# Optimization experiments

Measured on AMD Instinct MI355X. Metric: run time of the kernel, lower is better.

## Reference

```python
import jax, jax.numpy as jnp
import numpy as np

BN_EPS = 1e-5
MIN_DIST = 1e-10


def _conv_bn_relu(x, w, b, gamma, beta):
    # pointwise Conv1d (kernel=1) == per-point linear, then BatchNorm1d (training-mode
    # batch stats, biased variance, as torch does for normalization), then ReLU.
    y = jnp.einsum('oc,bcn->bon', w, x) + b[None, :, None]
    mu = y.mean(axis=(0, 2))
    var = y.var(axis=(0, 2))
    yn = (y - mu[None, :, None]) * jax.lax.rsqrt(var + BN_EPS)[None, :, None]
    return jax.nn.relu(yn * gamma[None, :, None] + beta[None, :, None])


def setup_inputs() -> dict:
    key = jax.random.key(0)
    ks = jax.random.split(key, 12)
    B, N1, N2, C1, C2 = 8, 8192, 2048, 128, 256
    in_ch = C1 + C2  # 384
    mlp = [256, 128]
    inp = {
        'xyz1': jax.random.normal(ks[0], (B, N1, 3), jnp.float32),
        'xyz2': jax.random.normal(ks[1], (B, N2, 3), jnp.float32),
        'points1': jax.random.normal(ks[2], (B, C1, N1), jnp.float32),
        'points2': jax.random.normal(ks[3], (B, C2, N2), jnp.float32),
    }
    last = in_ch
    for i, out_ch in enumerate(mlp):
        scale = 1.0 / np.sqrt(last)
        inp[f'w{i}'] = jax.random.uniform(ks[4 + 2 * i], (out_ch, last), jnp.float32, -scale, scale)
        inp[f'b{i}'] = jax.random.uniform(ks[5 + 2 * i], (out_ch,), jnp.float32, -scale, scale)
        inp[f'gamma{i}'] = jnp.ones((out_ch,), jnp.float32)
        inp[f'beta{i}'] = jnp.zeros((out_ch,), jnp.float32)
        last = out_ch
    return inp


def reference(xyz1, xyz2, points1, points2,
              w0, b0, gamma0, beta0, w1, b1, gamma1, beta1):
    # Euclidean distance matrix [B, N1, N2] (torch.cdist, p=2)
    sq = (jnp.sum(xyz1 * xyz1, -1)[:, :, None]
          + jnp.sum(xyz2 * xyz2, -1)[:, None, :]
          - 2.0 * jnp.einsum('bnd,bmd->bnm', xyz1, xyz2))
    dists = jnp.sqrt(jnp.maximum(sq, 0.0))
    # 3 smallest distances + indices (ascending, matching torch.topk largest=False)
    neg_d, knn_idx = jax.lax.top_k(-dists, 3)  # [B, N1, 3]
    knn_d = jnp.maximum(-neg_d, MIN_DIST)
    weights = 1.0 / knn_d
    weights = weights / jnp.sum(weights, axis=2, keepdims=True)  # [B, N1, 3]
    # gather neighbor features: points2 [B, C2, N2] -> [B, C2, N1, 3]
    knn_feats = jnp.take_along_axis(points2[:, :, None, :],
                                    knn_idx[:, None, :, :], axis=3)
    interpolated = jnp.sum(knn_feats * weights[:, None, :, :], axis=3)  # [B, C2, N1]
    new_points = jnp.concatenate([points1, interpolated], axis=1)  # [B, C1+C2, N1]
    new_points = _conv_bn_relu(new_points, w0, b0, gamma0, beta0)
    new_points = _conv_bn_relu(new_points, w1, b1, gamma1, beta1)
    return new_points
```

## Files before the change

### kernel.cpp

```cpp
#include <hip/hip_runtime.h>
#include <cstdint>

using u16 = unsigned short;
typedef short bf16x8 __attribute__((ext_vector_type(8)));
typedef float f32x4 __attribute__((ext_vector_type(4)));

__device__ __forceinline__ float bf2f(u16 h) {
    union { unsigned u; float f; } x;
    x.u = ((unsigned)h) << 16;
    return x.f;
}
__device__ __forceinline__ u16 f2bf(float f) {
    union { float f; unsigned u; } x;
    x.f = f;
    unsigned r = x.u + 0x7fffu + ((x.u >> 16) & 1u);
    return (u16)(r >> 16);
}

__device__ __forceinline__ void gl_lds16(const u16* g, u16* l) {
    __builtin_amdgcn_global_load_lds((const __attribute__((address_space(1))) void*)g,
                                     (__attribute__((address_space(3))) void*)l, 16, 0, 0);
}

#define N1 8192
#define N2 2048
#define C2 256

__global__ __launch_bounds__(256) void prep_misc(const float* __restrict__ w0,
                                                 const float* __restrict__ w1,
                                                 u16* __restrict__ w0b,
                                                 u16* __restrict__ w1b,
                                                 float* __restrict__ stats) {
    int bid = blockIdx.x, tid = threadIdx.x;
    if (bid < 384) {
        int i = bid * 256 + tid;
        w0b[i] = f2bf(w0[i]);
    } else if (bid < 512) {
        int i = (bid - 384) * 256 + tid;
        w1b[i] = f2bf(w1[i]);
    } else {
        for (int i = tid; i < 768; i += 256) stats[i] = 0.0f;
    }
}

__global__ __launch_bounds__(256) void transpose_to_bf16(const float* __restrict__ src,
                                                         u16* __restrict__ dst,
                                                         int C, int N, int dst_stride,
                                                         int col_off) {
    __shared__ float tile[32][33];
    int b = blockIdx.z;
    int n0 = blockIdx.x * 32, c0 = blockIdx.y * 32;
    int tx = threadIdx.x & 31, ty = threadIdx.x >> 5;
    const float* s = src + (long)b * C * N;
#pragma unroll
    for (int i = 0; i < 4; i++) {
        int c = ty + i * 8;
        tile[c][tx] = s[(long)(c0 + c) * N + n0 + tx];
    }
    __syncthreads();
    u16* d = dst + (long)b * N * dst_stride;
#pragma unroll
    for (int i = 0; i < 4; i++) {
        int n = ty + i * 8;
        d[(long)(n0 + n) * dst_stride + col_off + c0 + tx] = f2bf(tile[tx][n]);
    }
}

__global__ __launch_bounds__(256) void knn_interp(const float* __restrict__ xyz1,
                                                  const float* __restrict__ xyz2,
                                                  const u16* __restrict__ P2T,
                                                  u16* __restrict__ X) {
    __shared__ float4 pts[N2];
    __shared__ float m_d[4][64][3];
    __shared__ int   m_i[4][64][3];
    __shared__ int   s_idx[64][3];
    __shared__ float s_w[64][3];
    int b = blockIdx.y;
    int n0 = blockIdx.x * 64;
    int tid = threadIdx.x;
    int ql = tid & 63;
    int part = tid >> 6;

    for (int j = tid; j < N2; j += 256) {
        float x = xyz2[((long)b * N2 + j) * 3 + 0];
        float y = xyz2[((long)b * N2 + j) * 3 + 1];
        float z = xyz2[((long)b * N2 + j) * 3 + 2];
        float nsq = __fadd_rn(__fadd_rn(__fmul_rn(x, x), __fmul_rn(y, y)), __fmul_rn(z, z));
        pts[j] = make_float4(x, y, z, nsq);
    }
    __syncthreads();

    int n = n0 + ql;
    float px = xyz1[((long)b * N1 + n) * 3 + 0];
    float py = xyz1[((long)b * N1 + n) * 3 + 1];
    float pz = xyz1[((long)b * N1 + n) * 3 + 2];
    float psq = __fadd_rn(__fadd_rn(__fmul_rn(px, px), __fmul_rn(py, py)), __fmul_rn(pz, pz));

    float b0 = 1e30f, b1 = 1e30f, b2 = 1e30f;
    int i0 = 0, i1 = 0, i2 = 0;
    int jbeg = part * (N2 / 4);
#pragma unroll 8
    for (int jj = 0; jj < N2 / 4; jj++) {
        int j = jbeg + jj;
        float4 p = pts[j];
        float dot = __fadd_rn(__fadd_rn(__fmul_rn(px, p.x), __fmul_rn(py, p.y)),
                              __fmul_rn(pz, p.z));
        float sq = __fsub_rn(__fadd_rn(psq, p.w), __fmul_rn(2.0f, dot));
        if (sq < b2) {
            if (sq < b1) {
                b2 = b1; i2 = i1;
                if (sq < b0) { b1 = b0; i1 = i0; b0 = sq; i0 = j; }
                else         { b1 = sq; i1 = j; }
            } else { b2 = sq; i2 = j; }
        }
    }
    m_d[part][ql][0] = b0; m_d[part][ql][1] = b1; m_d[part][ql][2] = b2;
    m_i[part][ql][0] = i0; m_i[part][ql][1] = i1; m_i[part][ql][2] = i2;
    __syncthreads();

    if (tid < 64) {
        float c0 = 1e30f, c1 = 1e30f, c2 = 1e30f;
        int a0 = 0x7fffffff, a1 = 0x7fffffff, a2 = 0x7fffffff;
#pragma unroll
        for (int pp = 0; pp < 4; pp++) {
#pragma unroll
            for (int k = 0; k < 3; k++) {
                float d = m_d[pp][tid][k];
                int ix = m_i[pp][tid][k];
                if (d < c2 || (d == c2 && ix < a2)) {
                    if (d < c1 || (d == c1 && ix < a1)) {
                        c2 = c1; a2 = a1;
                        if (d < c0 || (d == c0 && ix < a0)) { c1 = c0; a1 = a0; c0 = d; a0 = ix; }
                        else                                { c1 = d; a1 = ix; }
                    } else { c2 = d; a2 = ix; }
                }
            }
        }
        float e0 = sqrtf(fmaxf(c0, 0.0f));
        float e1 = sqrtf(fmaxf(c1, 0.0f));
        float e2 = sqrtf(fmaxf(c2, 0.0f));
        float kd0 = fmaxf(e0, 1e-10f), kd1 = fmaxf(e1, 1e-10f), kd2 = fmaxf(e2, 1e-10f);
        float w0 = __fdiv_rn(1.0f, kd0), w1 = __fdiv_rn(1.0f, kd1), w2 = __fdiv_rn(1.0f, kd2);
        float wsum = __fadd_rn(__fadd_rn(w0, w1), w2);
        s_idx[tid][0] = a0; s_idx[tid][1] = a1; s_idx[tid][2] = a2;
        s_w[tid][0] = __fdiv_rn(w0, wsum);
        s_w[tid][1] = __fdiv_rn(w1, wsum);
        s_w[tid][2] = __fdiv_rn(w2, wsum);
    }
    __syncthreads();

    int l = tid & 63;
    const u16* base = P2T + (long)b * N2 * C2;
    for (int p = part; p < 64; p += 4) {
        int j0 = s_idx[p][0], j1 = s_idx[p][1], j2 = s_idx[p][2];
        float f0 = s_w[p][0], f1 = s_w[p][1], f2 = s_w[p][2];
        ushort4 r0 = *(const ushort4*)&base[(long)j0 * C2 + l * 4];
        ushort4 r1 = *(const ushort4*)&base[(long)j1 * C2 + l * 4];
        ushort4 r2 = *(const ushort4*)&base[(long)j2 * C2 + l * 4];
        ushort4 o;
        o.x = f2bf(__fadd_rn(__fadd_rn(__fmul_rn(bf2f(r0.x), f0), __fmul_rn(bf2f(r1.x), f1)),
                             __fmul_rn(bf2f(r2.x), f2)));
        o.y = f2bf(__fadd_rn(__fadd_rn(__fmul_rn(bf2f(r0.y), f0), __fmul_rn(bf2f(r1.y), f1)),
                             __fmul_rn(bf2f(r2.y), f2)));
        o.z = f2bf(__fadd_rn(__fadd_rn(__fmul_rn(bf2f(r0.z), f0), __fmul_rn(bf2f(r1.z), f1)),
                             __fmul_rn(bf2f(r2.z), f2)));
        o.w = f2bf(__fadd_rn(__fadd_rn(__fmul_rn(bf2f(r0.w), f0), __fmul_rn(bf2f(r1.w), f1)),
                             __fmul_rn(bf2f(r2.w), f2)));
        *(ushort4*)&X[(long)(b * N1 + n0 + p) * 384 + 128 + l * 4] = o;
    }
}

template <int KDIM, bool BN_IN, bool ASYNC>
__global__ __launch_bounds__(256) void gemm_bn(const u16* __restrict__ A,
                                               const u16* __restrict__ Bw,
                                               const float* __restrict__ bias,
                                               const float* __restrict__ g_in_sum,
                                               const float* __restrict__ g_in_ssq,
                                               const float* __restrict__ gamma_in,
                                               const float* __restrict__ beta_in,
                                               u16* __restrict__ Yout, int Ntot,
                                               float* __restrict__ g_out_sum,
                                               float* __restrict__ g_out_ssq) {
    constexpr int LD = ASYNC ? 32 : 40;
    __shared__ __align__(16) u16 Al[128 * LD];
    __shared__ __align__(16) u16 Bl[128 * LD];
    __shared__ float s_stats[256];
    __shared__ float s_scale[BN_IN ? KDIM : 2];
    __shared__ float s_shift[BN_IN ? KDIM : 2];

    int tid = threadIdx.x;
    long s0 = (long)blockIdx.x * 128;
    int o0 = blockIdx.y * 128;

    s_stats[tid] = 0.0f;
    if constexpr (BN_IN) {
        for (int k = tid; k < KDIM; k += 256) {
            float mu = g_in_sum[k] * (1.0f / 65536.0f);
            float var = g_in_ssq[k] * (1.0f / 65536.0f) - mu * mu;
            float rs = rsqrtf(var + 1e-5f);
            float sc = gamma_in[k] * rs;
            s_scale[k] = sc;
            s_shift[k] = beta_in[k] - mu * sc;
        }
    }
    int wid = tid >> 6, lane = tid & 63;
    int wm = wid >> 1, wn = wid & 1;
    int q = lane >> 4, l16 = lane & 15;

    f32x4 acc[4][4];
#pragma unroll
    for (int mi = 0; mi < 4; mi++)
#pragma unroll
        for (int ni = 0; ni < 4; ni++) acc[mi][ni] = (f32x4){0.f, 0.f, 0.f, 0.f};

    int rbase0 = wid * 32;
    int rsub = lane >> 2;
    int colsw = (((lane & 3) ^ (rsub & 3)) << 3);
    const u16* gA0 = A + (s0 + rbase0 + rsub) * KDIM + colsw;
    const u16* gA1 = gA0 + (long)16 * KDIM;
    const u16* gB0 = Bw + (long)(o0 + rbase0 + rsub) * KDIM + colsw;
    const u16* gB1 = gB0 + (long)16 * KDIM;
    u16* lA0 = &Al[rbase0 * 32];
    u16* lA1 = &Al[(rbase0 + 16) * 32];
    u16* lB0 = &Bl[rbase0 * 32];
    u16* lB1 = &Bl[(rbase0 + 16) * 32];
    int qA = ASYNC ? (q ^ (l16 & 3)) : q;

    __syncthreads();

    for (int kt = 0; kt < KDIM; kt += 32) {
        if constexpr (ASYNC) {
            gl_lds16(gA0 + kt, lA0);
            gl_lds16(gA1 + kt, lA1);
            gl_lds16(gB0 + kt, lB0);
            gl_lds16(gB1 + kt, lB1);
        } else {
#pragma unroll
            for (int cc = 0; cc < 2; cc++) {
                int ci = tid + cc * 256;
                int row = ci >> 2;
                int kc = (ci & 3) << 3;
                union { uint4 u; u16 h[8]; } va;
                va.u = *(const uint4*)(A + (s0 + row) * KDIM + kt + kc);
                if constexpr (BN_IN) {
#pragma unroll
                    for (int j = 0; j < 8; j++) {
                        float f = bf2f(va.h[j]);
                        f = fmaxf(fmaf(f, s_scale[kt + kc + j], s_shift[kt + kc + j]), 0.0f);
                        va.h[j] = f2bf(f);
                    }
                }
                *(uint4*)&Al[row * LD + kc] = va.u;
                *(uint4*)&Bl[row * LD + kc] = *(const uint4*)(Bw + (long)(o0 + row) * KDIM + kt + kc);
            }
        }
        __syncthreads();
        bf16x8 af[4], bfr[4];
#pragma unroll
        for (int mi = 0; mi < 4; mi++)
            af[mi] = *(const bf16x8*)&Al[(wm * 64 + mi * 16 + l16) * LD + qA * 8];
#pragma unroll
        for (int ni = 0; ni < 4; ni++)
            bfr[ni] = *(const bf16x8*)&Bl[(wn * 64 + ni * 16 + l16) * LD + qA * 8];
#pragma unroll
        for (int mi = 0; mi < 4; mi++)
#pragma unroll
            for (int ni = 0; ni < 4; ni++)
                acc[mi][ni] = __builtin_amdgcn_mfma_f32_16x16x32_bf16(af[mi], bfr[ni],
                                                                      acc[mi][ni], 0, 0, 0);
        __syncthreads();
    }

#pragma unroll
    for (int ni = 0; ni < 4; ni++) {
        int coll = wn * 64 + ni * 16 + l16;
        int col = o0 + coll;
        float bz = bias[col];
        float s1 = 0.0f, s2 = 0.0f;
#pragma unroll
        for (int mi = 0; mi < 4; mi++) {
#pragma unroll
            for (int r = 0; r < 4; r++) {
                float v = acc[mi][ni][r] + bz;
                s1 += v;
                s2 += v * v;
                long row = s0 + wm * 64 + mi * 16 + q * 4 + r;
                Yout[row * Ntot + col] = f2bf(v);
            }
        }
        s1 += __shfl_xor(s1, 16, 64);
        s1 += __shfl_xor(s1, 32, 64);
        s2 += __shfl_xor(s2, 16, 64);
        s2 += __shfl_xor(s2, 32, 64);
        if (q == 0) {
            atomicAdd(&s_stats[coll], s1);
            atomicAdd(&s_stats[128 + coll], s2);
        }
    }
    __syncthreads();
    if (tid < 128) {
        atomicAdd(&g_out_sum[o0 + tid], s_stats[tid]);
        atomicAdd(&g_out_ssq[o0 + tid], s_stats[128 + tid]);
    }
}

__global__ __launch_bounds__(256) void finalize_k(const u16* __restrict__ Y1,
                                                  const float* __restrict__ g_sum,
                                                  const float* __restrict__ g_ssq,
                                                  const float* __restrict__ gamma,
                                                  const float* __restrict__ beta,
                                                  float* __restrict__ out) {
    __shared__ float s_scale[128], s_shift[128];
    int tid = threadIdx.x;
    if (tid < 128) {
        float mu = g_sum[tid] * (1.0f / 65536.0f);
        float var = g_ssq[tid] * (1.0f / 65536.0f) - mu * mu;
        float rs = rsqrtf(var + 1e-5f);
        float sc = gamma[tid] * rs;
        s_scale[tid] = sc;
        s_shift[tid] = beta[tid] - mu * sc;
    }
    __syncthreads();
    long s = (long)blockIdx.x * 256 + tid;
    int b = (int)(s >> 13);
    int n = (int)(s & 8191);
    const u16* yrow = Y1 + s * 128;
    float* obase = out + (long)b * 128 * 8192 + n;
#pragma unroll
    for (int oc = 0; oc < 128; oc += 8) {
        union { uint4 u; u16 h[8]; } va;
        va.u = *(const uint4*)&yrow[oc];
#pragma unroll
        for (int k = 0; k < 8; k++) {
            int o = oc + k;
            float v = fmaxf(fmaf(bf2f(va.h[k]), s_scale[o], s_shift[o]), 0.0f);
            obase[(long)o * 8192] = v;
        }
    }
}

extern "C" void kernel_launch(void* const* d_in, const int* in_sizes, int n_in,
                              void* d_out, int out_size, void* d_ws, size_t ws_size,
                              hipStream_t stream) {
    const float* xyz1    = (const float*)d_in[0];
    const float* xyz2    = (const float*)d_in[1];
    const float* points1 = (const float*)d_in[2];
    const float* points2 = (const float*)d_in[3];
    const float* w0 = (const float*)d_in[4];
    const float* b0 = (const float*)d_in[5];
    const float* gamma0 = (const float*)d_in[6];
    const float* beta0 = (const float*)d_in[7];
    const float* w1 = (const float*)d_in[8];
    const float* b1 = (const float*)d_in[9];
    const float* gamma1 = (const float*)d_in[10];
    const float* beta1 = (const float*)d_in[11];
    float* out = (float*)d_out;

    char* ws = (char*)d_ws;
    u16* X       = (u16*)(ws + 0);
    u16* P2T     = (u16*)(ws + 50331648);
    u16* w0b     = (u16*)(ws + 58720256);
    u16* w1b     = (u16*)(ws + 58916864);
    u16* Y0      = (u16*)(ws + 58982400);
    u16* Y1b     = (u16*)(ws + 92536832);
    float* stats = (float*)(ws + 109314048);
    if (ws_size < 109317120) return;
    float* gsum0 = stats;
    float* gss0  = stats + 256;
    float* gsum1 = stats + 512;
    float* gss1  = stats + 640;

    prep_misc<<<513, 256, 0, stream>>>(w0, w1, w0b, w1b, stats);
    transpose_to_bf16<<<dim3(256, 4, 8), 256, 0, stream>>>(points1, X, 128, 8192, 384, 0);
    transpose_to_bf16<<<dim3(64, 8, 8), 256, 0, stream>>>(points2, P2T, 256, 2048, 256, 0);
    knn_interp<<<dim3(128, 8), 256, 0, stream>>>(xyz1, xyz2, P2T, X);
    gemm_bn<384, false, true><<<dim3(512, 2), 256, 0, stream>>>(
        X, w0b, b0, nullptr, nullptr, nullptr, nullptr, Y0, 256, gsum0, gss0);
    gemm_bn<256, true, false><<<dim3(512, 1), 256, 0, stream>>>(
        Y0, w1b, b1, gsum0, gss0, gamma0, beta0, Y1b, 128, gsum1, gss1);
    finalize_k<<<256, 256, 0, stream>>>(Y1b, gsum1, gss1, gamma1, beta1, out);
}
```

Measured before the change: 268.2 us.

## Fuse preprocessing kernels, halve knn LDS footprint, swap GEMM grid order

Merges the weight conversion, stats zeroing and both transposes into one preproc launch, which removes two kernel launches and their gaps. The knn kernel now stages xyz2 in two halves, halving its LDS use so more blocks can be resident per CU, at the cost of extra barriers. The GEMM grids are transposed so the two output-channel tiles for the same row block run next to each other, which should improve L2 reuse of the A tile. Tie-breaking in the knn merge is unchanged because each part still scans indices in ascending order.

```diff
diff --git a/kernel.cpp b/kernel.cpp
--- a/kernel.cpp
+++ b/kernel.cpp
@@ -26,43 +26,52 @@
 #define N2 2048
 #define C2 256
 
-__global__ __launch_bounds__(256) void prep_misc(const float* __restrict__ w0,
-                                                 const float* __restrict__ w1,
-                                                 u16* __restrict__ w0b,
-                                                 u16* __restrict__ w1b,
-                                                 float* __restrict__ stats) {
+__device__ __forceinline__ void tr_tile(const float* __restrict__ src,
+                                        u16* __restrict__ dst,
+                                        int C, int N, int ds, int b, int n0, int c0,
+                                        int tid, float (*tile)[33]) {
+    int tx = tid & 31, ty = tid >> 5;
+    const float* s = src + (long)b * C * N;
+#pragma unroll
+    for (int i = 0; i < 4; i++) {
+        int c = ty + i * 8;
+        tile[c][tx] = s[(long)(c0 + c) * N + n0 + tx];
+    }
+    __syncthreads();
+    u16* d = dst + (long)b * N * ds;
+#pragma unroll
+    for (int i = 0; i < 4; i++) {
+        int n = ty + i * 8;
+        d[(long)(n0 + n) * ds + c0 + tx] = f2bf(tile[tx][n]);
+    }
+}
+
+__global__ __launch_bounds__(256) void preproc(const float* __restrict__ w0,
+                                               const float* __restrict__ w1,
+                                               const float* __restrict__ points1,
+                                               const float* __restrict__ points2,
+                                               u16* __restrict__ w0b,
+                                               u16* __restrict__ w1b,
+                                               u16* __restrict__ X,
+                                               u16* __restrict__ P2T,
+                                               float* __restrict__ stats) {
+    __shared__ float tile[32][33];
     int bid = blockIdx.x, tid = threadIdx.x;
-    if (bid < 384) {
-        int i = bid * 256 + tid;
+    if (bid < 8192) {
+        int nb = bid & 255, cb = (bid >> 8) & 3, b = bid >> 10;
+        tr_tile(points1, X, 128, 8192, 384, b, nb * 32, cb * 32, tid, tile);
+    } else if (bid < 12288) {
+        int t = bid - 8192;
+        int nb = t & 63, cb = (t >> 6) & 7, b = t >> 9;
+        tr_tile(points2, P2T, 256, 2048, 256, b, nb * 32, cb * 32, tid, tile);
+    } else if (bid < 12672) {
+        int i = (bid - 12288) * 256 + tid;
         w0b[i] = f2bf(w0[i]);
-    } else if (bid < 512) {
-        int i = (bid - 384) * 256 + tid;
+    } else if (bid < 12800) {
+        int i = (bid - 12672) * 256 + tid;
         w1b[i] = f2bf(w1[i]);
     } else {
         for (int i = tid; i < 768; i += 256) stats[i] = 0.0f;
-    }
-}
-
-__global__ __launch_bounds__(256) void transpose_to_bf16(const float* __restrict__ src,
-                                                         u16* __restrict__ dst,
-                                                         int C, int N, int dst_stride,
-                                                         int col_off) {
-    __shared__ float tile[32][33];
-    int b = blockIdx.z;
-    int n0 = blockIdx.x * 32, c0 = blockIdx.y * 32;
-    int tx = threadIdx.x & 31, ty = threadIdx.x >> 5;
-    const float* s = src + (long)b * C * N;
-#pragma unroll
-    for (int i = 0; i < 4; i++) {
-        int c = ty + i * 8;
-        tile[c][tx] = s[(long)(c0 + c) * N + n0 + tx];
-    }
-    __syncthreads();
-    u16* d = dst + (long)b * N * dst_stride;
-#pragma unroll
-    for (int i = 0; i < 4; i++) {
-        int n = ty + i * 8;
-        d[(long)(n0 + n) * dst_stride + col_off + c0 + tx] = f2bf(tile[tx][n]);
     }
 }
 
@@ -70,7 +79,7 @@
                                                   const float* __restrict__ xyz2,
                                                   const u16* __restrict__ P2T,
                                                   u16* __restrict__ X) {
-    __shared__ float4 pts[N2];
+    __shared__ float4 pts[N2 / 2];
     __shared__ float m_d[4][64][3];
     __shared__ int   m_i[4][64][3];
     __shared__ int   s_idx[64][3];
@@ -81,15 +90,6 @@
     int ql = tid & 63;
     int part = tid >> 6;
 
-    for (int j = tid; j < N2; j += 256) {
-        float x = xyz2[((long)b * N2 + j) * 3 + 0];
-        float y = xyz2[((long)b * N2 + j) * 3 + 1];
-        float z = xyz2[((long)b * N2 + j) * 3 + 2];
-        float nsq = __fadd_rn(__fadd_rn(__fmul_rn(x, x), __fmul_rn(y, y)), __fmul_rn(z, z));
-        pts[j] = make_float4(x, y, z, nsq);
-    }
-    __syncthreads();
-
     int n = n0 + ql;
     float px = xyz1[((long)b * N1 + n) * 3 + 0];
     float py = xyz1[((long)b * N1 + n) * 3 + 1];
@@ -98,21 +98,36 @@
 
     float b0 = 1e30f, b1 = 1e30f, b2 = 1e30f;
     int i0 = 0, i1 = 0, i2 = 0;
-    int jbeg = part * (N2 / 4);
+
+    for (int half = 0; half < 2; half++) {
+        for (int j = tid; j < N2 / 2; j += 256) {
+            int jg = half * (N2 / 2) + j;
+            float x = xyz2[((long)b * N2 + jg) * 3 + 0];
+            float y = xyz2[((long)b * N2 + jg) * 3 + 1];
+            float z = xyz2[((long)b * N2 + jg) * 3 + 2];
+            float nsq = __fadd_rn(__fadd_rn(__fmul_rn(x, x), __fmul_rn(y, y)), __fmul_rn(z, z));
+            pts[j] = make_float4(x, y, z, nsq);
+        }
+        __syncthreads();
+
+        int jbeg = half * (N2 / 2) + part * (N2 / 8);
+        const float4* lp = &pts[part * (N2 / 8)];
 #pragma unroll 8
-    for (int jj = 0; jj < N2 / 4; jj++) {
-        int j = jbeg + jj;
-        float4 p = pts[j];
-        float dot = __fadd_rn(__fadd_rn(__fmul_rn(px, p.x), __fmul_rn(py, p.y)),
-                              __fmul_rn(pz, p.z));
-        float sq = __fsub_rn(__fadd_rn(psq, p.w), __fmul_rn(2.0f, dot));
-        if (sq < b2) {
-            if (sq < b1) {
-                b2 = b1; i2 = i1;
-                if (sq < b0) { b1 = b0; i1 = i0; b0 = sq; i0 = j; }
-                else         { b1 = sq; i1 = j; }
-            } else { b2 = sq; i2 = j; }
-        }
+        for (int jj = 0; jj < N2 / 8; jj++) {
+            int j = jbeg + jj;
+            float4 p = lp[jj];
+            float dot = __fadd_rn(__fadd_rn(__fmul_rn(px, p.x), __fmul_rn(py, p.y)),
+                                  __fmul_rn(pz, p.z));
+            float sq = __fsub_rn(__fadd_rn(psq, p.w), __fmul_rn(2.0f, dot));
+            if (sq < b2) {
+                if (sq < b1) {
+                    b2 = b1; i2 = i1;
+                    if (sq < b0) { b1 = b0; i1 = i0; b0 = sq; i0 = j; }
+                    else         { b1 = sq; i1 = j; }
+                } else { b2 = sq; i2 = j; }
+            }
+        }
+        __syncthreads();
     }
     m_d[part][ql][0] = b0; m_d[part][ql][1] = b1; m_d[part][ql][2] = b2;
     m_i[part][ql][0] = i0; m_i[part][ql][1] = i1; m_i[part][ql][2] = i2;
@@ -189,8 +204,8 @@
     __shared__ float s_shift[BN_IN ? KDIM : 2];
 
     int tid = threadIdx.x;
-    long s0 = (long)blockIdx.x * 128;
-    int o0 = blockIdx.y * 128;
+    long s0 = (long)blockIdx.y * 128;
+    int o0 = blockIdx.x * 128;
 
     s_stats[tid] = 0.0f;
     if constexpr (BN_IN) {
@@ -370,13 +385,11 @@
     float* gsum1 = stats + 512;
     float* gss1  = stats + 640;
 
-    prep_misc<<<513, 256, 0, stream>>>(w0, w1, w0b, w1b, stats);
-    transpose_to_bf16<<<dim3(256, 4, 8), 256, 0, stream>>>(points1, X, 128, 8192, 384, 0);
-    transpose_to_bf16<<<dim3(64, 8, 8), 256, 0, stream>>>(points2, P2T, 256, 2048, 256, 0);
+    preproc<<<12801, 256, 0, stream>>>(w0, w1, points1, points2, w0b, w1b, X, P2T, stats);
     knn_interp<<<dim3(128, 8), 256, 0, stream>>>(xyz1, xyz2, P2T, X);
-    gemm_bn<384, false, true><<<dim3(512, 2), 256, 0, stream>>>(
+    gemm_bn<384, false, true><<<dim3(2, 512), 256, 0, stream>>>(
         X, w0b, b0, nullptr, nullptr, nullptr, nullptr, Y0, 256, gsum0, gss0);
-    gemm_bn<256, true, false><<<dim3(512, 1), 256, 0, stream>>>(
+    gemm_bn<256, true, false><<<dim3(1, 512), 256, 0, stream>>>(
         Y0, w1b, b1, gsum0, gss0, gamma0, beta0, Y1b, 128, gsum1, gss1);
     finalize_k<<<256, 256, 0, stream>>>(Y1b, gsum1, gss1, gamma1, beta1, out);
 }
```

Measured after the change: 258.0 us. 3.8% less time.
